# Kernel tuning notes

Hardware: AMD Instinct MI355X
Metric: run time of the kernel (lower is better)

The kernel has to match this reference:

```python
import jax, jax.numpy as jnp
import numpy as np

B, T, IN = 128, 2048, 32      # batch, seq_len, input dim
S, M = 32, 8                  # kaarma state dim, number of ensemble models
E, H = 64, 128                # encoder dim, controller GRU hidden
CIN = E + 1                   # controller input = [encoded, error]


def setup_inputs() -> dict:
    key = jax.random.key(0)
    ks = jax.random.split(key, 15)
    sc = 0.1  # small init scale keeps tanh/sigmoid in sane range
    return {
        "x": jax.random.normal(ks[0], (B, T, IN), jnp.float32),
        "y": jax.random.normal(ks[1], (B, T), jnp.float32),
        # mkaarma params: shared encoder + per-model recurrent state update
        "W_enc": jax.random.normal(ks[2], (IN, E), jnp.float32) * sc,
        "b_enc": jnp.zeros((E,), jnp.float32),
        "W_in": jax.random.normal(ks[3], (M, IN, S), jnp.float32) * sc,
        "W_rec": jax.random.normal(ks[4], (M, S, S), jnp.float32) * sc,
        "b_s": jnp.zeros((M, S), jnp.float32),
        # controller params: GRU cell + gate head
        "W_x": jax.random.normal(ks[5], (CIN, 3 * H), jnp.float32) * sc,
        "W_h": jax.random.normal(ks[6], (H, 3 * H), jnp.float32) * sc,
        "b_x": jnp.zeros((3 * H,), jnp.float32),
        "b_h": jnp.zeros((3 * H,), jnp.float32),
        "W_gate": jax.random.normal(ks[7], (H, M), jnp.float32) * sc,
        "b_gate": jnp.zeros((M,), jnp.float32),
    }


def reference(x, y, W_enc, b_enc, W_in, W_rec, b_s,
              W_x, W_h, b_x, b_h, W_gate, b_gate):
    Bv = x.shape[0]
    dt = x.dtype

    def step(carry, xy):
        kstate, h, err = carry            # [B,S], [B,H], [B]
        x_t, y_t = xy                     # [B,IN], [B]
        # mkaarma: encode input + ensemble of candidate next states
        encoded = jnp.tanh(x_t @ W_enc + b_enc)                        # [B,E]
        new_state = jnp.tanh(
            jnp.einsum('bi,mis->bms', x_t, W_in)
            + jnp.einsum('bs,msd->bmd', kstate, W_rec)
            + b_s
        )                                                              # [B,M,S]
        # controller: GRU cell on [encoded, error]
        inp = jnp.concatenate([encoded, err[:, None]], axis=1)         # [B,E+1]
        xz, xr, xn = jnp.split(inp @ W_x + b_x, 3, axis=1)
        hz, hr, hn = jnp.split(h @ W_h + b_h, 3, axis=1)
        z = jax.nn.sigmoid(xz + hz)
        r = jax.nn.sigmoid(xr + hr)
        n = jnp.tanh(xn + r * hn)
        h_new = (1.0 - z) * n + z * h                                  # [B,H]
        # gate softmax over models, mix candidate states
        gate = jax.nn.softmax(h_new @ W_gate + b_gate, axis=1)         # [B,M]
        kstate_new = jnp.einsum('bm,bms->bs', gate, new_state)         # [B,S]
        pred = kstate_new[:, -1]                                       # [B]
        err_new = pred - y_t
        return (kstate_new, h_new, err_new), pred

    init = (jnp.zeros((Bv, S), dt), jnp.zeros((Bv, H), dt), jnp.zeros((Bv,), dt))
    xs = (jnp.swapaxes(x, 0, 1), jnp.swapaxes(y, 0, 1))   # time-major
    _, preds = jax.lax.scan(step, init, xs)               # [T,B]
    return jnp.swapaxes(preds, 0, 1)                      # [B,T]
```

## Files before the change

### kernel.cpp

```cpp
#include <hip/hip_runtime.h>

typedef _Float16 h2 __attribute__((ext_vector_type(2)));
typedef _Float16 h8 __attribute__((ext_vector_type(8)));

#define NB 128
#define NT 2048
#define NIN 32
#define NS 32
#define NM 8
#define NE 64
#define NH 128
#define NH3 384
#define RPW 16

__device__ __forceinline__ h2 mkh2(float a, float b) {
  h2 r; r[0] = (_Float16)a; r[1] = (_Float16)b; return r;
}

template <int I>
__device__ __forceinline__ h2 pick2(h8 v) {
  return __builtin_shufflevector(v, v, 2 * I, 2 * I + 1);
}

__device__ __forceinline__ float fdot2(h2 a, h2 b, float c) {
#if __has_builtin(__builtin_amdgcn_fdot2)
  return __builtin_amdgcn_fdot2(a, b, c, false);
#else
  return c + (float)a[0] * (float)b[0] + (float)a[1] * (float)b[1];
#endif
}

__device__ __forceinline__ float rcpf(float v) {
#if __has_builtin(__builtin_amdgcn_rcpf)
  return __builtin_amdgcn_rcpf(v);
#else
  return 1.0f / v;
#endif
}

__device__ __forceinline__ float sigmoid_f(float v) { return rcpf(1.0f + __expf(-v)); }
__device__ __forceinline__ float tanh_f(float v) { return 1.0f - 2.0f * rcpf(1.0f + __expf(2.0f * v)); }

__device__ __forceinline__ float f16bits_tof(unsigned short u) {
  _Float16 h;
  __builtin_memcpy(&h, &u, 2);
  return (float)h;
}

template <int CTRL>
__device__ __forceinline__ float dppadd(float v) {
  int t = __builtin_amdgcn_update_dpp(0, __float_as_int(v), CTRL, 0xF, 0xF, true);
  return v + __int_as_float(t);
}
__device__ __forceinline__ float wave_reduce63(float v) {
  v = dppadd<0x111>(v); v = dppadd<0x112>(v); v = dppadd<0x114>(v);
  v = dppadd<0x118>(v); v = dppadd<0x142>(v); v = dppadd<0x143>(v);
  return v;
}
__device__ __forceinline__ float pairsum(float v) {
  int t = __builtin_amdgcn_update_dpp(0, __float_as_int(v), 0xB1, 0xF, 0xF, true);
  return v + __int_as_float(t);
}

__device__ __forceinline__ void lds_fence() {
  asm volatile("s_waitcnt lgkmcnt(0)" ::: "memory");
}

__device__ __forceinline__ void waitflag(int* f) {
  while (__hip_atomic_load(f, __ATOMIC_ACQUIRE, __HIP_MEMORY_SCOPE_AGENT) == 0)
    __builtin_amdgcn_s_sleep(2);
}

__global__ __launch_bounds__(384, 1) void fused(
    const float* __restrict__ gx, const float* __restrict__ gy,
    const float* __restrict__ W_enc, const float* __restrict__ b_enc,
    const float* __restrict__ W_in, const float* __restrict__ W_rec,
    const float* __restrict__ b_s, const float* __restrict__ W_x,
    const float* __restrict__ W_h, const float* __restrict__ b_x,
    const float* __restrict__ b_h, const float* __restrict__ W_gate,
    const float* __restrict__ b_gate, _Float16* __restrict__ xpre,
    _Float16* __restrict__ xh16, float* __restrict__ out,
    float* __restrict__ state, int* __restrict__ flags, int t0, int CH) {
  const int tid = threadIdx.x;

  __shared__ __align__(16) _Float16 x16[4][NIN];
  __shared__ __align__(16) _Float16 encA[4][RPW][NE];
  __shared__ __align__(16) _Float16 h_sh[2][NH];
  __shared__ __align__(16) _Float16 xpre_sh[2][NH3];
  __shared__ __align__(16) float ns_sh[2][NS][NM];
  __shared__ __align__(16) float xd_sh[2][2 * NH];
  __shared__ __align__(16) float gp_sh[2][4][NM];
  __shared__ __align__(16) _Float16 kst_sh[NS];
  __shared__ float err_sh;
  __shared__ float y_lds[NT];

  if (blockIdx.x >= NB) {
    const int pb = (int)blockIdx.x - NB;
    const int bb = pb % NB;
    const int cc = pb / NB;
    if (tid < 256) {
      const int wv = tid >> 6, lane = tid & 63;
      h2 we[16];
#pragma unroll
      for (int i = 0; i < 16; ++i)
        we[i] = mkh2(W_enc[(2 * i) * NE + lane], W_enc[(2 * i + 1) * NE + lane]);
      const float be = b_enc[lane];
      const int tc0 = cc * 64 + wv * RPW;

      h2 wx3[96];
#pragma unroll 1
      for (int pass = 0; pass < 2; ++pass) {
#pragma unroll
        for (int kk = 0; kk < 3; ++kk) {
          const int j = lane + 64 * (3 * pass + kk);
#pragma unroll
          for (int i = 0; i < 32; ++i)
            wx3[kk * 32 + i] = mkh2(W_x[(size_t)(2 * i) * NH3 + j],
                                    W_x[(size_t)(2 * i + 1) * NH3 + j]);
        }
#pragma unroll 1
        for (int r = 0; r < RPW; ++r) {
          const int tc = tc0 + r;
          const size_t g = (size_t)bb * CH + tc;
          if (pass == 0) {
            const float* xr = gx + ((size_t)bb * NT + t0 + tc) * NIN;
            if (lane < NIN) x16[wv][lane] = (_Float16)xr[lane];
            lds_fence();
            if (lane < 16) {
              const unsigned v = *(const unsigned*)&x16[wv][2 * lane];
              ((unsigned*)xh16)[g * 16 + lane] = v;
            }
            const h8* xv8 = (const h8*)x16[wv];
            float a = be;
#pragma unroll
            for (int i = 0; i < 4; ++i) {
              const h8 xv = xv8[i];
              a = fdot2(pick2<0>(xv), we[4 * i + 0], a);
              a = fdot2(pick2<1>(xv), we[4 * i + 1], a);
              a = fdot2(pick2<2>(xv), we[4 * i + 2], a);
              a = fdot2(pick2<3>(xv), we[4 * i + 3], a);
            }
            encA[wv][r][lane] = (_Float16)tanh_f(a);
            lds_fence();
          }
          const h8* ev8 = (const h8*)encA[wv][r];
          h8 ev[8];
#pragma unroll
          for (int i = 0; i < 8; ++i) ev[i] = ev8[i];
#pragma unroll
          for (int kk = 0; kk < 3; ++kk) {
            const int j = lane + 64 * (3 * pass + kk);
            float a = b_x[j], c = 0.f;
#pragma unroll
            for (int i = 0; i < 8; ++i) {
              a = fdot2(pick2<0>(ev[i]), wx3[kk * 32 + 4 * i + 0], a);
              c = fdot2(pick2<1>(ev[i]), wx3[kk * 32 + 4 * i + 1], c);
              a = fdot2(pick2<2>(ev[i]), wx3[kk * 32 + 4 * i + 2], a);
              c = fdot2(pick2<3>(ev[i]), wx3[kk * 32 + 4 * i + 3], c);
            }
            xpre[g * NH3 + j] = (_Float16)(a + c);
          }
        }
      }
    }
    asm volatile("s_waitcnt vmcnt(0)" ::: "memory");
    __syncthreads();
    if (tid == 0) {
      __threadfence();
      __hip_atomic_store(&flags[pb], 1, __ATOMIC_RELEASE,
                         __HIP_MEMORY_SCOPE_AGENT);
    }
    return;
  }

  const int b = blockIdx.x;
  const int wv = tid >> 6;
  const int lane = tid & 63;

  float* st = state + b * (NH + NS + 1);

  h2 wbig[96];
  h2 wrec[16];
  float wg[8];
  float bh[3], wxe[3];
  float bs4[4];
  float bg[8];
  float h_prev = 0.f;
  unsigned xpq[12];
  h8 xr0[4], xr1[4], xr2[4], xr3[4];
  int readyf = -1;

  const int gl = tid - 128;
  const int j = gl >> 1;
  const int half = gl & 1;

  for (int i = tid; i < CH; i += 384) y_lds[i] = gy[(size_t)b * NT + t0 + i];

  if (wv >= 2) {
#pragma unroll
    for (int g = 0; g < 3; ++g) {
      const int jc = j + 128 * g;
#pragma unroll
      for (int i = 0; i < 32; ++i)
        wbig[g * 32 + i] = mkh2(W_h[(size_t)(64 * half + 2 * i) * NH3 + jc],
                                W_h[(size_t)(64 * half + 2 * i + 1) * NH3 + jc]);
      bh[g] = b_h[jc];
      wxe[g] = W_x[(size_t)NE * NH3 + jc];
    }
#pragma unroll
    for (int m = 0; m < 8; ++m) wg[m] = half ? 0.f : W_gate[j * NM + m];
    {
      const int m0 = gl >> 5, d0 = gl & 31;
#pragma unroll
      for (int i = 0; i < 16; ++i)
        wrec[i] = mkh2(W_rec[m0 * 1024 + (2 * i) * 32 + d0],
                       W_rec[m0 * 1024 + (2 * i + 1) * 32 + d0]);
    }
    h_prev = t0 ? st[j] : 0.f;
    if (!half) h_sh[1][j] = (_Float16)h_prev;
  } else if (wv == 1) {
#pragma unroll
    for (int k = 0; k < 4; ++k) {
      const int o = lane + 64 * k, m = o >> 5, d = o & 31;
#pragma unroll
      for (int i = 0; i < 16; ++i)
        wbig[k * 16 + i] = mkh2(W_in[m * 1024 + (2 * i) * 32 + d],
                                W_in[m * 1024 + (2 * i + 1) * 32 + d]);
      bs4[k] = b_s[o];
    }
    waitflag(&flags[b]);
    readyf = b;
    {
      const h8* x0 = (const h8*)(xh16 + (size_t)(b * CH) * NIN);
#pragma unroll
      for (int i = 0; i < 4; ++i) xr0[i] = x0[i];
#pragma unroll
      for (int k = 0; k < 4; ++k) {
        float s = bs4[k];
#pragma unroll
        for (int i = 0; i < 4; ++i) {
          s = fdot2(pick2<0>(xr0[i]), wbig[k * 16 + 4 * i + 0], s);
          s = fdot2(pick2<1>(xr0[i]), wbig[k * 16 + 4 * i + 1], s);
          s = fdot2(pick2<2>(xr0[i]), wbig[k * 16 + 4 * i + 2], s);
          s = fdot2(pick2<3>(xr0[i]), wbig[k * 16 + 4 * i + 3], s);
        }
        xd_sh[1][lane + 64 * k] = s;
      }
    }
  } else {
#pragma unroll
    for (int m = 0; m < 8; ++m) bg[m] = b_gate[m];
    if (lane < NS) kst_sh[lane] = t0 ? (_Float16)st[NH + lane] : (_Float16)0.f;
    if (lane == 0) err_sh = t0 ? st[NH + NS] : 0.f;
  }
  __syncthreads();

  float hz = 0.f, hr = 0.f, hn = 0.f;

#define STEPK(K, XRK)                                                          \
  {                                                                            \
    const int tc = tc4 + (K);                                                  \
    const int q = (K) & 1, qp = q ^ 1;                                         \
                                 \
    if (wv >= 2) {                                                             \
      const h8* hv8 = (const h8*)&h_sh[qp][64 * half];                         \
      float a0 = 0.f, c0 = 0.f, a1 = 0.f, c1 = 0.f, a2 = 0.f, c2 = 0.f;        \
      _Pragma("unroll")                                                        \
      for (int i = 0; i < 8; ++i) {                                            \
        const h8 hv = hv8[i];                                                  \
        a0 = fdot2(pick2<0>(hv), wbig[4 * i + 0], a0);                         \
        c0 = fdot2(pick2<1>(hv), wbig[4 * i + 1], c0);                         \
        a0 = fdot2(pick2<2>(hv), wbig[4 * i + 2], a0);                         \
        c0 = fdot2(pick2<3>(hv), wbig[4 * i + 3], c0);                         \
        a1 = fdot2(pick2<0>(hv), wbig[32 + 4 * i + 0], a1);                    \
        c1 = fdot2(pick2<1>(hv), wbig[32 + 4 * i + 1], c1);                    \
        a1 = fdot2(pick2<2>(hv), wbig[32 + 4 * i + 2], a1);                    \
        c1 = fdot2(pick2<3>(hv), wbig[32 + 4 * i + 3], c1);                    \
        a2 = fdot2(pick2<0>(hv), wbig[64 + 4 * i + 0], a2);                    \
        c2 = fdot2(pick2<1>(hv), wbig[64 + 4 * i + 1], c2);                    \
        a2 = fdot2(pick2<2>(hv), wbig[64 + 4 * i + 2], a2);                    \
        c2 = fdot2(pick2<3>(hv), wbig[64 + 4 * i + 3], c2);                    \
      }                                                                        \
      hz = pairsum(a0 + c0) + bh[0];                                           \
      hr = pairsum(a1 + c1) + bh[1];                                           \
      hn = pairsum(a2 + c2) + bh[2];                                           \
    } else if (wv == 0) {                                                      \
      if (tc > 0) {                                                            \
        const int u = lane & 31;                                               \
        const float4* nsv = (const float4*)&ns_sh[qp][u][0];                   \
        const float4 n0 = nsv[0], n1 = nsv[1];                                 \
        const float4* g4 = (const float4*)&gp_sh[qp][0][0];                    \
        float4 A = g4[0], Bv = g4[1];                                          \
        A.x += g4[2].x + g4[4].x + g4[6].x; A.y += g4[2].y + g4[4].y + g4[6].y;\
        A.z += g4[2].z + g4[4].z + g4[6].z; A.w += g4[2].w + g4[4].w + g4[6].w;\
        Bv.x += g4[3].x + g4[5].x + g4[7].x; Bv.y += g4[3].y + g4[5].y + g4[7].y;\
        Bv.z += g4[3].z + g4[5].z + g4[7].z; Bv.w += g4[3].w + g4[5].w + g4[7].w;\
        float l[8] = {A.x + bg[0], A.y + bg[1], A.z + bg[2], A.w + bg[3],      \
                      Bv.x + bg[4], Bv.y + bg[5], Bv.z + bg[6], Bv.w + bg[7]}; \
        float mx = fmaxf(fmaxf(fmaxf(l[0], l[1]), fmaxf(l[2], l[3])),          \
                         fmaxf(fmaxf(l[4], l[5]), fmaxf(l[6], l[7])));         \
        float e[8], s = 0.f;                                                   \
        _Pragma("unroll")                                                      \
        for (int m = 0; m < 8; ++m) { e[m] = __expf(l[m] - mx); s += e[m]; }   \
        float ks = e[0] * n0.x + e[1] * n0.y + e[2] * n0.z + e[3] * n0.w +     \
                   e[4] * n1.x + e[5] * n1.y + e[6] * n1.z + e[7] * n1.w;      \
        ks *= rcpf(s);                                                         \
        if (lane < NS) kst_sh[u] = (_Float16)ks;                               \
        if (lane == 31) {                                                      \
          out[(size_t)b * NT + t0 + tc - 1] = ks;                              \
          err_sh = ks - y_lds[tc - 1];                                         \
        }                                                                      \
      }                                                                        \
    } else {              \
      if ((K) == 0) {                                                          \
        const int needf = (min(tc4 + 8, CH - 1) >> 6) * NB + b;                \
        if (needf > readyf) { waitflag(&flags[needf]); readyf = needf; }       \
        const unsigned* xpg = (const unsigned*)xpre;                           \
        _Pragma("unroll")                                                      \
        for (int k = 0; k < 4; ++k) {                                          \
          const size_t rr = (size_t)(b * CH + tc4 + k) * 192;                  \
          xpq[3 * k + 0] = xpg[rr + lane];                                     \
          xpq[3 * k + 1] = xpg[rr + lane + 64];                                \
          xpq[3 * k + 2] = xpg[rr + lane + 128];                               \
        }                                                                      \
        const h8* xg0 = (const h8*)(xh16 + (size_t)(b * CH + min(tc4 + 1, CH - 1)) * NIN); \
        const h8* xg1 = (const h8*)(xh16 + (size_t)(b * CH + min(tc4 + 2, CH - 1)) * NIN); \
        const h8* xg2 = (const h8*)(xh16 + (size_t)(b * CH + min(tc4 + 3, CH - 1)) * NIN); \
        const h8* xg3 = (const h8*)(xh16 + (size_t)(b * CH + min(tc4 + 4, CH - 1)) * NIN); \
        _Pragma("unroll")                                                      \
        for (int i = 0; i < 4; ++i) {                                          \
          xr0[i] = xg0[i]; xr1[i] = xg1[i]; xr2[i] = xg2[i]; xr3[i] = xg3[i];  \
        }                                                                      \
      }                                                                        \
      unsigned* xps = (unsigned*)&xpre_sh[q][0];                               \
      xps[lane] = xpq[3 * (K) + 0];                                            \
      xps[lane + 64] = xpq[3 * (K) + 1];                                       \
      xps[lane + 128] = xpq[3 * (K) + 2];                                      \
    }                                                                          \
    __syncthreads();                                                           \
                                 \
    if (wv >= 2) {                                                             \
      const float err = err_sh;                                                \
      const float xz = (float)xpre_sh[q][j] + err * wxe[0];                    \
      const float xr = (float)xpre_sh[q][j + 128] + err * wxe[1];              \
      const float xn = (float)xpre_sh[q][j + 256] + err * wxe[2];              \
      const float z = sigmoid_f(hz + xz);                                      \
      const float r = sigmoid_f(hr + xr);                                      \
      const float n = tanh_f(xn + r * hn);                                     \
      const float hnew = (1.f - z) * n + z * h_prev;                           \
      h_prev = hnew;                                                           \
      if (!half) h_sh[q][j] = (_Float16)hnew;                                  \
      float p[8];                                                              \
      _Pragma("unroll")                                                        \
      for (int m = 0; m < 8; ++m) p[m] = wave_reduce63(hnew * wg[m]);          \
      if (lane == 63) {                                                        \
        *(float4*)&gp_sh[q][wv - 2][0] = make_float4(p[0], p[1], p[2], p[3]);  \
        *(float4*)&gp_sh[q][wv - 2][4] = make_float4(p[4], p[5], p[6], p[7]);  \
      }                                                                        \
      const h8* kv8 = (const h8*)kst_sh;                                       \
      float s = xd_sh[qp][gl];                                                 \
      _Pragma("unroll")                                                        \
      for (int i = 0; i < 4; ++i) {                                            \
        const h8 kv = kv8[i];                                                  \
        s = fdot2(pick2<0>(kv), wrec[4 * i + 0], s);                           \
        s = fdot2(pick2<1>(kv), wrec[4 * i + 1], s);                           \
        s = fdot2(pick2<2>(kv), wrec[4 * i + 2], s);                           \
        s = fdot2(pick2<3>(kv), wrec[4 * i + 3], s);                           \
      }                                                                        \
      ns_sh[q][gl & 31][gl >> 5] = tanh_f(s);                                  \
    } else if (wv == 1) {                                                      \
      if (tc + 1 < CH) {                                                       \
        _Pragma("unroll")                                                      \
        for (int k = 0; k < 4; ++k) {                                          \
          float s = bs4[k];                                                    \
          _Pragma("unroll")                                                    \
          for (int i = 0; i < 4; ++i) {                                        \
            s = fdot2(pick2<0>(XRK[i]), wbig[k * 16 + 4 * i + 0], s);          \
            s = fdot2(pick2<1>(XRK[i]), wbig[k * 16 + 4 * i + 1], s);          \
            s = fdot2(pick2<2>(XRK[i]), wbig[k * 16 + 4 * i + 2], s);          \
            s = fdot2(pick2<3>(XRK[i]), wbig[k * 16 + 4 * i + 3], s);          \
          }                                                                    \
          xd_sh[q][lane + 64 * k] = s;                                         \
        }                                                                      \
      }                                                                        \
    }                                                                          \
    __syncthreads();                                                           \
  }

  for (int tc4 = 0; tc4 < CH; tc4 += 4) {
    STEPK(0, xr0)
    STEPK(1, xr1)
    STEPK(2, xr2)
    STEPK(3, xr3)
  }
#undef STEPK

  if (wv == 0) {
    const int qf = (CH - 1) & 1;
    const int u = lane & 31;
    const float4* nsv = (const float4*)&ns_sh[qf][u][0];
    const float4 n0 = nsv[0], n1 = nsv[1];
    const float4* g4 = (const float4*)&gp_sh[qf][0][0];
    float4 A = g4[0], Bv = g4[1];
    A.x += g4[2].x + g4[4].x + g4[6].x; A.y += g4[2].y + g4[4].y + g4[6].y;
    A.z += g4[2].z + g4[4].z + g4[6].z; A.w += g4[2].w + g4[4].w + g4[6].w;
    Bv.x += g4[3].x + g4[5].x + g4[7].x; Bv.y += g4[3].y + g4[5].y + g4[7].y;
    Bv.z += g4[3].z + g4[5].z + g4[7].z; Bv.w += g4[3].w + g4[5].w + g4[7].w;
    float l[8] = {A.x + bg[0], A.y + bg[1], A.z + bg[2], A.w + bg[3],
                  Bv.x + bg[4], Bv.y + bg[5], Bv.z + bg[6], Bv.w + bg[7]};
    float mx = fmaxf(fmaxf(fmaxf(l[0], l[1]), fmaxf(l[2], l[3])),
                     fmaxf(fmaxf(l[4], l[5]), fmaxf(l[6], l[7])));
    float e[8], s = 0.f;
#pragma unroll
    for (int m = 0; m < 8; ++m) { e[m] = __expf(l[m] - mx); s += e[m]; }
    float ks = e[0] * n0.x + e[1] * n0.y + e[2] * n0.z + e[3] * n0.w +
               e[4] * n1.x + e[5] * n1.y + e[6] * n1.z + e[7] * n1.w;
    ks *= rcpf(s);
    if (lane < NS) st[NH + u] = ks;
    if (lane == 31) {
      out[(size_t)b * NT + t0 + CH - 1] = ks;
      st[NH + NS] = ks - y_lds[CH - 1];
    }
  }
  if (wv >= 2 && !half) st[j] = h_prev;
}

extern "C" void kernel_launch(void* const* d_in, const int* in_sizes, int n_in,
                              void* d_out, int out_size, void* d_ws, size_t ws_size,
                              hipStream_t stream) {
  const float* x = (const float*)d_in[0];
  const float* y = (const float*)d_in[1];
  const float* W_enc = (const float*)d_in[2];
  const float* b_enc = (const float*)d_in[3];
  const float* W_in = (const float*)d_in[4];
  const float* W_rec = (const float*)d_in[5];
  const float* b_s = (const float*)d_in[6];
  const float* W_x = (const float*)d_in[7];
  const float* W_h = (const float*)d_in[8];
  const float* b_x = (const float*)d_in[9];
  const float* b_h = (const float*)d_in[10];
  const float* W_gate = (const float*)d_in[11];
  const float* b_gate = (const float*)d_in[12];
  float* out = (float*)d_out;

  const size_t stateB = (size_t)NB * (NH + NS + 1) * sizeof(float);
  int CH = NT;
  while (CH > 64) {
    const size_t need = (size_t)NB * CH * NH3 * 2 + (size_t)NB * CH * NIN * 2 +
                        stateB + (size_t)(NB * CH / 64) * sizeof(int);
    if (need <= ws_size) break;
    CH >>= 1;
  }
  const int npre = NB * CH / 64;

  _Float16* xpre = (_Float16*)d_ws;
  _Float16* xh16 = (_Float16*)((char*)d_ws + (size_t)NB * CH * NH3 * 2);
  float* state = (float*)((char*)d_ws + (size_t)NB * CH * NH3 * 2 +
                          (size_t)NB * CH * NIN * 2);
  int* flags = (int*)((char*)state + stateB);

  for (int t0 = 0; t0 < NT; t0 += CH) {
    (void)hipMemsetAsync(flags, 0, (size_t)npre * sizeof(int), stream);
    fused<<<dim3(NB + npre), dim3(384), 0, stream>>>(
        x, y, W_enc, b_enc, W_in, W_rec, b_s, W_x, W_h, b_x, b_h, W_gate,
        b_gate, xpre, xh16, out, state, flags, t0, CH);
  }
}
```

Before: 2.525 ms.

## Double producer rows per wave and prefetch inputs in the xpre producer

Producer blocks now cover 128 timesteps each, with 32 rows per wave instead of 16. This halves the number of producer blocks and spreads each register load of the W_x slice over twice as many rows. The pass loop is split so pass 0 prefetches the next x row into a register and pass 1 double-buffers the encoded row from LDS. The encoder dot product is also split into two accumulator chains to shorten the dependency chain. In exchange, the first flag a consumer waits on becomes ready later, and each producer wave holds more registers.

```diff
diff --git a/kernel.cpp b/kernel.cpp
--- a/kernel.cpp
+++ b/kernel.cpp
@@ -11,7 +11,7 @@
 #define NE 64
 #define NH 128
 #define NH3 384
-#define RPW 16
+#define RPW 32
 
 __device__ __forceinline__ h2 mkh2(float a, float b) {
   h2 r; r[0] = (_Float16)a; r[1] = (_Float16)b; return r;
@@ -105,9 +105,10 @@
       for (int i = 0; i < 16; ++i)
         we[i] = mkh2(W_enc[(2 * i) * NE + lane], W_enc[(2 * i + 1) * NE + lane]);
       const float be = b_enc[lane];
-      const int tc0 = cc * 64 + wv * RPW;
+      const int tc0 = cc * 128 + wv * RPW;
 
       h2 wx3[96];
+      float bx3[3];
 #pragma unroll 1
       for (int pass = 0; pass < 2; ++pass) {
 #pragma unroll
@@ -117,48 +118,81 @@
           for (int i = 0; i < 32; ++i)
             wx3[kk * 32 + i] = mkh2(W_x[(size_t)(2 * i) * NH3 + j],
                                     W_x[(size_t)(2 * i + 1) * NH3 + j]);
+          bx3[kk] = b_x[j];
         }
+        if (pass == 0) {
+          float xreg = 0.f;
+          if (lane < NIN) xreg = gx[((size_t)bb * NT + t0 + tc0) * NIN + lane];
 #pragma unroll 1
-        for (int r = 0; r < RPW; ++r) {
-          const int tc = tc0 + r;
-          const size_t g = (size_t)bb * CH + tc;
-          if (pass == 0) {
-            const float* xr = gx + ((size_t)bb * NT + t0 + tc) * NIN;
-            if (lane < NIN) x16[wv][lane] = (_Float16)xr[lane];
+          for (int r = 0; r < RPW; ++r) {
+            const int tc = tc0 + r;
+            const size_t g = (size_t)bb * CH + tc;
+            if (lane < NIN) x16[wv][lane] = (_Float16)xreg;
+            if (r + 1 < RPW && lane < NIN)
+              xreg = gx[((size_t)bb * NT + t0 + tc + 1) * NIN + lane];
             lds_fence();
             if (lane < 16) {
               const unsigned v = *(const unsigned*)&x16[wv][2 * lane];
               ((unsigned*)xh16)[g * 16 + lane] = v;
             }
             const h8* xv8 = (const h8*)x16[wv];
-            float a = be;
+            float a = be, c = 0.f;
 #pragma unroll
             for (int i = 0; i < 4; ++i) {
               const h8 xv = xv8[i];
               a = fdot2(pick2<0>(xv), we[4 * i + 0], a);
-              a = fdot2(pick2<1>(xv), we[4 * i + 1], a);
+              c = fdot2(pick2<1>(xv), we[4 * i + 1], c);
               a = fdot2(pick2<2>(xv), we[4 * i + 2], a);
-              a = fdot2(pick2<3>(xv), we[4 * i + 3], a);
+              c = fdot2(pick2<3>(xv), we[4 * i + 3], c);
             }
-            encA[wv][r][lane] = (_Float16)tanh_f(a);
+            encA[wv][r][lane] = (_Float16)tanh_f(a + c);
             lds_fence();
+            const h8* ev8 = (const h8*)encA[wv][r];
+            h8 ev[8];
+#pragma unroll
+            for (int i = 0; i < 8; ++i) ev[i] = ev8[i];
+#pragma unroll
+            for (int kk = 0; kk < 3; ++kk) {
+              float a0 = bx3[kk], c0 = 0.f;
+#pragma unroll
+              for (int i = 0; i < 8; ++i) {
+                a0 = fdot2(pick2<0>(ev[i]), wx3[kk * 32 + 4 * i + 0], a0);
+                c0 = fdot2(pick2<1>(ev[i]), wx3[kk * 32 + 4 * i + 1], c0);
+                a0 = fdot2(pick2<2>(ev[i]), wx3[kk * 32 + 4 * i + 2], a0);
+                c0 = fdot2(pick2<3>(ev[i]), wx3[kk * 32 + 4 * i + 3], c0);
+              }
+              xpre[g * NH3 + lane + 64 * kk] = (_Float16)(a0 + c0);
+            }
           }
-          const h8* ev8 = (const h8*)encA[wv][r];
-          h8 ev[8];
-#pragma unroll
-          for (int i = 0; i < 8; ++i) ev[i] = ev8[i];
-#pragma unroll
-          for (int kk = 0; kk < 3; ++kk) {
-            const int j = lane + 64 * (3 * pass + kk);
-            float a = b_x[j], c = 0.f;
-#pragma unroll
-            for (int i = 0; i < 8; ++i) {
-              a = fdot2(pick2<0>(ev[i]), wx3[kk * 32 + 4 * i + 0], a);
-              c = fdot2(pick2<1>(ev[i]), wx3[kk * 32 + 4 * i + 1], c);
-              a = fdot2(pick2<2>(ev[i]), wx3[kk * 32 + 4 * i + 2], a);
-              c = fdot2(pick2<3>(ev[i]), wx3[kk * 32 + 4 * i + 3], c);
+        } else {
+          h8 ev[8], evn[8];
+          {
+            const h8* e8 = (const h8*)encA[wv][0];
+#pragma unroll
+            for (int i = 0; i < 8; ++i) ev[i] = e8[i];
+          }
+#pragma unroll 1
+          for (int r = 0; r < RPW; ++r) {
+            if (r + 1 < RPW) {
+              const h8* e8 = (const h8*)encA[wv][r + 1];
+#pragma unroll
+              for (int i = 0; i < 8; ++i) evn[i] = e8[i];
             }
-            xpre[g * NH3 + j] = (_Float16)(a + c);
+            const size_t g = (size_t)bb * CH + tc0 + r;
+#pragma unroll
+            for (int kk = 0; kk < 3; ++kk) {
+              float a0 = bx3[kk], c0 = 0.f;
+#pragma unroll
+              for (int i = 0; i < 8; ++i) {
+                a0 = fdot2(pick2<0>(ev[i]), wx3[kk * 32 + 4 * i + 0], a0);
+                c0 = fdot2(pick2<1>(ev[i]), wx3[kk * 32 + 4 * i + 1], c0);
+                a0 = fdot2(pick2<2>(ev[i]), wx3[kk * 32 + 4 * i + 2], a0);
+                c0 = fdot2(pick2<3>(ev[i]), wx3[kk * 32 + 4 * i + 3], c0);
+              }
+              xpre[g * NH3 + lane + 64 * (3 + kk)] = (_Float16)(a0 + c0);
+            }
+#pragma unroll
+            for (int i = 0; i < 8; ++i) ev[i] = evn[i];
           }
         }
       }
@@ -313,7 +347,7 @@
       }                                                                        \
     } else {              \
       if ((K) == 0) {                                                          \
-        const int needf = (min(tc4 + 8, CH - 1) >> 6) * NB + b;                \
+        const int needf = (min(tc4 + 8, CH - 1) >> 7) * NB + b;                \
         if (needf > readyf) { waitflag(&flags[needf]); readyf = needf; }       \
         const unsigned* xpg = (const unsigned*)xpre;                           \
         _Pragma("unroll")                                                      \
@@ -445,13 +479,13 @@
 
   const size_t stateB = (size_t)NB * (NH + NS + 1) * sizeof(float);
   int CH = NT;
-  while (CH > 64) {
+  while (CH > 128) {
     const size_t need = (size_t)NB * CH * NH3 * 2 + (size_t)NB * CH * NIN * 2 +
-                        stateB + (size_t)(NB * CH / 64) * sizeof(int);
+                        stateB + (size_t)(NB * CH / 128) * sizeof(int);
     if (need <= ws_size) break;
     CH >>= 1;
   }
-  const int npre = NB * CH / 64;
+  const int npre = NB * CH / 128;
 
   _Float16* xpre = (_Float16*)d_ws;
   _Float16* xh16 = (_Float16*)((char*)d_ws + (size_t)NB * CH * NH3 * 2);
```

Result: slower. 2.578 ms (+2.1%).
